# Kernel optimization log

Measured on AMD Instinct MI355X. Metric: run time of the kernel, lower is better.

## Reference

```python
import jax, jax.numpy as jnp
import numpy as np

N_NODES = 50000
N_EDGES = 800000
D = 128            # embedding.hidden_size == sage.hidden_channels
SYN_V, LEM_V, POS_V, SEN_V = 120000, 150000, 5, 210000
LN_EPS = 1e-12


def setup_inputs() -> dict:
    key = jax.random.key(0)
    ks = jax.random.split(key, 12)
    s = 0.02
    inp = {
        "x": jax.random.randint(ks[0], (N_NODES, 4), 0, 5, dtype=jnp.int64)
             if jax.config.jax_enable_x64 else jax.random.randint(ks[0], (N_NODES, 4), 0, 5, dtype=jnp.int32),
        "edge_index": jax.random.randint(ks[1], (2, N_EDGES), 0, N_NODES, dtype=jnp.int32),
        "syn_emb": jax.random.normal(ks[2], (SYN_V, D), jnp.float32) * s,
        "lem_emb": jax.random.normal(ks[3], (LEM_V, D), jnp.float32) * s,
        "pos_emb": jax.random.normal(ks[4], (POS_V, D), jnp.float32) * s,
        "sen_emb": jax.random.normal(ks[5], (SEN_V, D), jnp.float32) * s,
        "ln_g": jnp.ones((D,), jnp.float32),
        "ln_b": jnp.zeros((D,), jnp.float32),
        "Wl0": jax.random.normal(ks[6], (D, D), jnp.float32) * s,
        "bl0": jnp.zeros((D,), jnp.float32),
        "Wr0": jax.random.normal(ks[7], (D, D), jnp.float32) * s,
        "Wl1": jax.random.normal(ks[8], (D, D), jnp.float32) * s,
        "bl1": jnp.zeros((D,), jnp.float32),
        "Wr1": jax.random.normal(ks[9], (D, D), jnp.float32) * s,
    }
    return inp


def _layer_norm(h, g, b):
    mu = jnp.mean(h, axis=-1, keepdims=True)
    var = jnp.mean(jnp.square(h - mu), axis=-1, keepdims=True)
    return (h - mu) * jax.lax.rsqrt(var + LN_EPS) * g + b


def _sage_conv(h, src, dst, Wl, bl, Wr, n_nodes):
    # mean-aggregate source neighbor features at each target node
    msg = h[src]                                            # [E, D] gather
    agg = jax.ops.segment_sum(msg, dst, num_segments=n_nodes)
    cnt = jax.ops.segment_sum(jnp.ones((src.shape[0],), h.dtype), dst,
                              num_segments=n_nodes)
    agg = agg / jnp.maximum(cnt, 1.0)[:, None]              # isolated nodes -> 0
    return agg @ Wl.T + bl + h @ Wr.T                       # lin_l(agg)+lin_r(x)


def reference(x, edge_index, syn_emb, lem_emb, pos_emb, sen_emb, ln_g, ln_b,
              Wl0, bl0, Wr0, Wl1, bl1, Wr1):
    # WordnetEmbeddings: sum of 4 lookups, LayerNorm (dropout = eval identity)
    h = (syn_emb[x[:, 0]] + lem_emb[x[:, 3]]
         + pos_emb[x[:, 1]] + sen_emb[x[:, 2]])
    h = _layer_norm(h, ln_g, ln_b)
    src, dst = edge_index[0], edge_index[1]
    n = h.shape[0]
    # SAGE.full_forward, 2 layers, relu between (dropout = eval identity)
    h = _sage_conv(h, src, dst, Wl0, bl0, Wr0, n)
    h = jax.nn.relu(h)
    h = _sage_conv(h, src, dst, Wl1, bl1, Wr1, n)
    return h
```

## Files before the change

### kernel.cpp

```cpp
#include <hip/hip_runtime.h>

#define D 128
#define LN_EPS 1e-12f

typedef unsigned int uint;
typedef unsigned short ushort_t;
typedef __attribute__((ext_vector_type(8))) short bf16x8;
typedef __attribute__((ext_vector_type(4))) float f32x4;

__device__ inline ushort_t f2bf(float f) {
  uint u = __float_as_uint(f);
  u += 0x7fffu + ((u >> 16) & 1u);
  return (ushort_t)(u >> 16);
}
__device__ inline float bf2f(ushort_t h) {
  return __uint_as_float((uint)h << 16);
}
__device__ inline uint pack_bf16(float a, float b) {
  return (uint)f2bf(a) | ((uint)f2bf(b) << 16);
}

__global__ __launch_bounds__(256) void front_kernel(
    const int* __restrict__ x,
    const float* __restrict__ syn, const float* __restrict__ lem,
    const float* __restrict__ pos, const float* __restrict__ sen,
    const float* __restrict__ g, const float* __restrict__ b,
    ushort_t* __restrict__ hH, ushort_t* __restrict__ hL, int n,
    const int* __restrict__ dst, int* __restrict__ counts, int nEdges,
    const float* __restrict__ Wl0, const float* __restrict__ Wr0,
    const float* __restrict__ Wl1, const float* __restrict__ Wr1,
    ushort_t* __restrict__ Wb0H, ushort_t* __restrict__ Wb0L,
    ushort_t* __restrict__ Wb1H, ushort_t* __restrict__ Wb1L,
    int embB, int histB) {
  int blk = blockIdx.x;
  if (blk >= embB + histB) {
    int idx = (blk - embB - histB) * 256 + threadIdx.x;
    int layer = idx >> 15;
    int e = idx & 32767;
    int col = e >> 8, k = e & 255;
    const float* Wl = layer ? Wl1 : Wl0;
    const float* Wr = layer ? Wr1 : Wr0;
    float v = (k < 128) ? Wl[col * 128 + k] : Wr[col * 128 + (k - 128)];
    ushort_t h = f2bf(v);
    float lo = v - bf2f(h);
    if (layer) {
      Wb1H[e] = h; Wb1L[e] = f2bf(lo);
    } else {
      Wb0H[e] = h; Wb0L[e] = f2bf(lo);
    }
    return;
  }
  if (blk >= embB) {
    int e = (blk - embB) * 256 + threadIdx.x;
    if (e < nEdges) atomicAdd(&counts[dst[e]], 1);
    return;
  }
  int lane = threadIdx.x & 63;
  int q = lane & 31, s = lane >> 5;
  int node = blk * 8 + (threadIdx.x >> 6) * 2 + s;
  if (node >= n) return;
  int4 xi = ((const int4*)x)[node];
  float4 v0 = ((const float4*)(syn + (size_t)xi.x * D))[q];
  float4 v1 = ((const float4*)(pos + (size_t)xi.y * D))[q];
  float4 v2 = ((const float4*)(sen + (size_t)xi.z * D))[q];
  float4 v3 = ((const float4*)(lem + (size_t)xi.w * D))[q];
  float4 hs;
  hs.x = v0.x + v1.x + v2.x + v3.x;
  hs.y = v0.y + v1.y + v2.y + v3.y;
  hs.z = v0.z + v1.z + v2.z + v3.z;
  hs.w = v0.w + v1.w + v2.w + v3.w;
  float sum = hs.x + hs.y + hs.z + hs.w;
#pragma unroll
  for (int off = 16; off; off >>= 1) sum += __shfl_xor(sum, off);
  float mu = sum * (1.0f / 128.0f);
  float4 d;
  d.x = hs.x - mu; d.y = hs.y - mu; d.z = hs.z - mu; d.w = hs.w - mu;
  float sq = d.x * d.x + d.y * d.y + d.z * d.z + d.w * d.w;
#pragma unroll
  for (int off = 16; off; off >>= 1) sq += __shfl_xor(sq, off);
  float rstd = rsqrtf(sq * (1.0f / 128.0f) + LN_EPS);
  float4 gg = ((const float4*)g)[q];
  float4 bb = ((const float4*)b)[q];
  float4 o;
  o.x = d.x * rstd * gg.x + bb.x;
  o.y = d.y * rstd * gg.y + bb.y;
  o.z = d.z * rstd * gg.z + bb.z;
  o.w = d.w * rstd * gg.w + bb.w;
  ushort_t hx = f2bf(o.x), hy = f2bf(o.y), hz = f2bf(o.z), hw = f2bf(o.w);
  uint2 ph;
  ph.x = (uint)hx | ((uint)hy << 16);
  ph.y = (uint)hz | ((uint)hw << 16);
  ((uint2*)(hH + (size_t)node * D))[q] = ph;
  uint2 pl;
  pl.x = pack_bf16(o.x - bf2f(hx), o.y - bf2f(hy));
  pl.y = pack_bf16(o.z - bf2f(hz), o.w - bf2f(hw));
  ((uint2*)(hL + (size_t)node * D))[q] = pl;
}

__global__ __launch_bounds__(256) void scan_part_kernel(
    const int* __restrict__ counts, int* __restrict__ partials) {
  int t = threadIdx.x;
  int base = blockIdx.x * 1024 + t * 4;
  int4 v = *(const int4*)(counts + base);
  int s = v.x + v.y + v.z + v.w;
#pragma unroll
  for (int off = 1; off < 64; off <<= 1) s += __shfl_xor(s, off);
  __shared__ int ws[4];
  if ((t & 63) == 0) ws[t >> 6] = s;
  __syncthreads();
  if (t == 0) partials[blockIdx.x] = ws[0] + ws[1] + ws[2] + ws[3];
}

__global__ __launch_bounds__(256) void scan_write_kernel(
    const int* __restrict__ counts, const int* __restrict__ partials,
    int* __restrict__ row_ptr, int n, int E) {
  int t = threadIdx.x;
  int b = blockIdx.x;
  int off = 0;
  for (int i = 0; i < b; ++i) off += partials[i];
  int base = b * 1024 + t * 4;
  int4 v = *(const int4*)(counts + base);
  int s = v.x + v.y + v.z + v.w;
  int lane = t & 63;
  int incl = s;
#pragma unroll
  for (int dd = 1; dd < 64; dd <<= 1) {
    int u = __shfl_up(incl, dd);
    if (lane >= dd) incl += u;
  }
  __shared__ int wsum[4];
  if (lane == 63) wsum[t >> 6] = incl;
  __syncthreads();
  int wid = t >> 6;
  int wpre = 0;
#pragma unroll
  for (int w = 0; w < 4; ++w)
    if (w < wid) wpre += wsum[w];
  int excl = off + wpre + incl - s;
  int4 r;
  r.x = excl;
  r.y = excl + v.x;
  r.z = r.y + v.y;
  r.w = r.z + v.z;
  if (base + 3 < n) {
    *(int4*)(row_ptr + base) = r;
  } else {
    if (base < n) row_ptr[base] = r.x;
    if (base + 1 < n) row_ptr[base + 1] = r.y;
    if (base + 2 < n) row_ptr[base + 2] = r.z;
    if (base + 3 < n) row_ptr[base + 3] = r.w;
  }
  if (b == 0 && t == 0) row_ptr[n] = E;
}

__global__ __launch_bounds__(256) void fill_kernel(const int* __restrict__ src,
                                                   const int* __restrict__ dst,
                                                   const int* __restrict__ row_ptr,
                                                   int* __restrict__ cursor,
                                                   int* __restrict__ adj,
                                                   int nEdges) {
  int e = blockIdx.x * 256 + threadIdx.x;
  if (e >= nEdges) return;
  int d = dst[e];
  int p = atomicAdd(&cursor[d], 1);
  adj[row_ptr[d] + p] = src[e];
}

__global__ __launch_bounds__(256) void gather_bf16_kernel(
    const int* __restrict__ row_ptr, const int* __restrict__ adj,
    const ushort_t* __restrict__ hb,
    ushort_t* __restrict__ aggH, ushort_t* __restrict__ aggL, int n) {
  int node = blockIdx.x * 4 + (threadIdx.x >> 6);
  if (node >= n) return;
  int lane = threadIdx.x & 63;
  int q = lane & 15, s = lane >> 4;
  int beg = row_ptr[node], end = row_ptr[node + 1];
  int count = end - beg;
  float a0 = 0.f, a1 = 0.f, a2 = 0.f, a3 = 0.f;
  float a4 = 0.f, a5 = 0.f, a6 = 0.f, a7 = 0.f;
  int lim16 = beg + (count & ~15);
  for (int bb = beg; bb < lim16; bb += 16) {
    int e0 = adj[bb + s];
    int e1 = adj[bb + 4 + s];
    int e2 = adj[bb + 8 + s];
    int e3 = adj[bb + 12 + s];
    uint4 v0 = ((const uint4*)(hb + (size_t)e0 * D))[q];
    uint4 v1 = ((const uint4*)(hb + (size_t)e1 * D))[q];
    uint4 v2 = ((const uint4*)(hb + (size_t)e2 * D))[q];
    uint4 v3 = ((const uint4*)(hb + (size_t)e3 * D))[q];
    a0 += __uint_as_float(v0.x << 16) + __uint_as_float(v1.x << 16) +
          __uint_as_float(v2.x << 16) + __uint_as_float(v3.x << 16);
    a1 += __uint_as_float(v0.x & 0xffff0000u) + __uint_as_float(v1.x & 0xffff0000u) +
          __uint_as_float(v2.x & 0xffff0000u) + __uint_as_float(v3.x & 0xffff0000u);
    a2 += __uint_as_float(v0.y << 16) + __uint_as_float(v1.y << 16) +
          __uint_as_float(v2.y << 16) + __uint_as_float(v3.y << 16);
    a3 += __uint_as_float(v0.y & 0xffff0000u) + __uint_as_float(v1.y & 0xffff0000u) +
          __uint_as_float(v2.y & 0xffff0000u) + __uint_as_float(v3.y & 0xffff0000u);
    a4 += __uint_as_float(v0.z << 16) + __uint_as_float(v1.z << 16) +
          __uint_as_float(v2.z << 16) + __uint_as_float(v3.z << 16);
    a5 += __uint_as_float(v0.z & 0xffff0000u) + __uint_as_float(v1.z & 0xffff0000u) +
          __uint_as_float(v2.z & 0xffff0000u) + __uint_as_float(v3.z & 0xffff0000u);
    a6 += __uint_as_float(v0.w << 16) + __uint_as_float(v1.w << 16) +
          __uint_as_float(v2.w << 16) + __uint_as_float(v3.w << 16);
    a7 += __uint_as_float(v0.w & 0xffff0000u) + __uint_as_float(v1.w & 0xffff0000u) +
          __uint_as_float(v2.w & 0xffff0000u) + __uint_as_float(v3.w & 0xffff0000u);
  }
  int p = lim16;
  if (count & 8) {
    int e0 = adj[p + s], e1 = adj[p + 4 + s];
    uint4 v0 = ((const uint4*)(hb + (size_t)e0 * D))[q];
    uint4 v1 = ((const uint4*)(hb + (size_t)e1 * D))[q];
    a0 += __uint_as_float(v0.x << 16) + __uint_as_float(v1.x << 16);
    a1 += __uint_as_float(v0.x & 0xffff0000u) + __uint_as_float(v1.x & 0xffff0000u);
    a2 += __uint_as_float(v0.y << 16) + __uint_as_float(v1.y << 16);
    a3 += __uint_as_float(v0.y & 0xffff0000u) + __uint_as_float(v1.y & 0xffff0000u);
    a4 += __uint_as_float(v0.z << 16) + __uint_as_float(v1.z << 16);
    a5 += __uint_as_float(v0.z & 0xffff0000u) + __uint_as_float(v1.z & 0xffff0000u);
    a6 += __uint_as_float(v0.w << 16) + __uint_as_float(v1.w << 16);
    a7 += __uint_as_float(v0.w & 0xffff0000u) + __uint_as_float(v1.w & 0xffff0000u);
    p += 8;
  }
  for (int i = p + s; i < end; i += 4) {
    int e0 = adj[i];
    uint4 v0 = ((const uint4*)(hb + (size_t)e0 * D))[q];
    a0 += __uint_as_float(v0.x << 16);
    a1 += __uint_as_float(v0.x & 0xffff0000u);
    a2 += __uint_as_float(v0.y << 16);
    a3 += __uint_as_float(v0.y & 0xffff0000u);
    a4 += __uint_as_float(v0.z << 16);
    a5 += __uint_as_float(v0.z & 0xffff0000u);
    a6 += __uint_as_float(v0.w << 16);
    a7 += __uint_as_float(v0.w & 0xffff0000u);
  }
#pragma unroll
  for (int off = 16; off <= 32; off <<= 1) {
    a0 += __shfl_xor(a0, off); a1 += __shfl_xor(a1, off);
    a2 += __shfl_xor(a2, off); a3 += __shfl_xor(a3, off);
    a4 += __shfl_xor(a4, off); a5 += __shfl_xor(a5, off);
    a6 += __shfl_xor(a6, off); a7 += __shfl_xor(a7, off);
  }
  if (s == 0) {
    float inv = 1.0f / fmaxf((float)count, 1.0f);
    float v0 = a0 * inv, v1 = a1 * inv, v2 = a2 * inv, v3 = a3 * inv;
    float v4 = a4 * inv, v5 = a5 * inv, v6 = a6 * inv, v7 = a7 * inv;
    ushort_t h0 = f2bf(v0), h1 = f2bf(v1), h2 = f2bf(v2), h3 = f2bf(v3);
    ushort_t h4 = f2bf(v4), h5 = f2bf(v5), h6 = f2bf(v6), h7 = f2bf(v7);
    uint4 ph;
    ph.x = (uint)h0 | ((uint)h1 << 16);
    ph.y = (uint)h2 | ((uint)h3 << 16);
    ph.z = (uint)h4 | ((uint)h5 << 16);
    ph.w = (uint)h6 | ((uint)h7 << 16);
    uint4 pl;
    pl.x = pack_bf16(v0 - bf2f(h0), v1 - bf2f(h1));
    pl.y = pack_bf16(v2 - bf2f(h2), v3 - bf2f(h3));
    pl.z = pack_bf16(v4 - bf2f(h4), v5 - bf2f(h5));
    pl.w = pack_bf16(v6 - bf2f(h6), v7 - bf2f(h7));
    *(uint4*)(aggH + (size_t)node * D + q * 8) = ph;
    *(uint4*)(aggL + (size_t)node * D + q * 8) = pl;
  }
}

__global__ __launch_bounds__(256) void sage_mfma_kernel(
    const ushort_t* __restrict__ aggH, const ushort_t* __restrict__ aggL,
    const ushort_t* hinH, const ushort_t* hinL,
    const ushort_t* __restrict__ WbH, const ushort_t* __restrict__ WbL,
    const float* __restrict__ bias,
    float* outF, ushort_t* outH, ushort_t* outL, int n, int doRelu) {
  __shared__ ushort_t AsH[128 * 64];
  __shared__ ushort_t AsL[128 * 64];
  __shared__ ushort_t BsH[128 * 64];
  __shared__ ushort_t BsL[128 * 64];
  int tid = threadIdx.x;
  int lane = tid & 63;
  int wave = tid >> 6;
  int base = blockIdx.x * 128;
  int wr = (wave & 1) * 64;
  int wc = (wave >> 1) * 64;

  f32x4 zero = {0.f, 0.f, 0.f, 0.f};
  f32x4 acc[4][4];
#pragma unroll
  for (int i = 0; i < 4; ++i)
#pragma unroll
    for (int j = 0; j < 4; ++j) acc[i][j] = zero;

  int row = tid >> 1;
  int half = tid & 1;
  int kb0 = half * 64;
  int swz = (row & 7) << 4;
  char* aHdst = (char*)AsH + row * 128;
  char* aLdst = (char*)AsL + row * 128;
  char* bHdst = (char*)BsH + row * 128;
  char* bLdst = (char*)BsL + row * 128;
  int anode = base + row;
  if (anode >= n) anode = n - 1;
  const ushort_t* wHsrc = WbH + (size_t)row * 256 + half * 32;
  const ushort_t* wLsrc = WbL + (size_t)row * 256 + half * 32;

  for (int kc = 0; kc < 4; ++kc) {
    {
      const ushort_t* sH = (kc < 2 ? aggH : hinH) +
                           (size_t)anode * D + (kc & 1) * 64 + half * 32;
      const ushort_t* sL = (kc < 2 ? aggL : hinL) +
                           (size_t)anode * D + (kc & 1) * 64 + half * 32;
      uint4 h0 = *(const uint4*)sH;
      uint4 h1 = *(const uint4*)(sH + 8);
      uint4 h2 = *(const uint4*)(sH + 16);
      uint4 h3 = *(const uint4*)(sH + 24);
      uint4 l0 = *(const uint4*)sL;
      uint4 l1 = *(const uint4*)(sL + 8);
      uint4 l2 = *(const uint4*)(sL + 16);
      uint4 l3 = *(const uint4*)(sL + 24);
      *(uint4*)(aHdst + ((kb0) ^ swz)) = h0;
      *(uint4*)(aHdst + ((kb0 + 16) ^ swz)) = h1;
      *(uint4*)(aHdst + ((kb0 + 32) ^ swz)) = h2;
      *(uint4*)(aHdst + ((kb0 + 48) ^ swz)) = h3;
      *(uint4*)(aLdst + ((kb0) ^ swz)) = l0;
      *(uint4*)(aLdst + ((kb0 + 16) ^ swz)) = l1;
      *(uint4*)(aLdst + ((kb0 + 32) ^ swz)) = l2;
      *(uint4*)(aLdst + ((kb0 + 48) ^ swz)) = l3;
    }
    {
      const ushort_t* sH = wHsrc + kc * 64;
      const ushort_t* sL = wLsrc + kc * 64;
      uint4 h0 = *(const uint4*)sH;
      uint4 h1 = *(const uint4*)(sH + 8);
      uint4 h2 = *(const uint4*)(sH + 16);
      uint4 h3 = *(const uint4*)(sH + 24);
      uint4 l0 = *(const uint4*)sL;
      uint4 l1 = *(const uint4*)(sL + 8);
      uint4 l2 = *(const uint4*)(sL + 16);
      uint4 l3 = *(const uint4*)(sL + 24);
      *(uint4*)(bHdst + ((kb0) ^ swz)) = h0;
      *(uint4*)(bHdst + ((kb0 + 16) ^ swz)) = h1;
      *(uint4*)(bHdst + ((kb0 + 32) ^ swz)) = h2;
      *(uint4*)(bHdst + ((kb0 + 48) ^ swz)) = h3;
      *(uint4*)(bLdst + ((kb0) ^ swz)) = l0;
      *(uint4*)(bLdst + ((kb0 + 16) ^ swz)) = l1;
      *(uint4*)(bLdst + ((kb0 + 32) ^ swz)) = l2;
      *(uint4*)(bLdst + ((kb0 + 48) ^ swz)) = l3;
    }
    __syncthreads();
#pragma unroll
    for (int ks = 0; ks < 2; ++ks) {
      int kb = ks * 64 + (lane >> 4) * 16;
      bf16x8 aHf[4], aLf[4], bHf[4], bLf[4];
#pragma unroll
      for (int rf = 0; rf < 4; ++rf) {
        int r = wr + rf * 16 + (lane & 15);
        int off = r * 128 + (kb ^ ((r & 7) << 4));
        aHf[rf] = *(const bf16x8*)((const char*)AsH + off);
        aLf[rf] = *(const bf16x8*)((const char*)AsL + off);
      }
#pragma unroll
      for (int cf = 0; cf < 4; ++cf) {
        int c = wc + cf * 16 + (lane & 15);
        int off = c * 128 + (kb ^ ((c & 7) << 4));
        bHf[cf] = *(const bf16x8*)((const char*)BsH + off);
        bLf[cf] = *(const bf16x8*)((const char*)BsL + off);
      }
#pragma unroll
      for (int rf = 0; rf < 4; ++rf)
#pragma unroll
        for (int cf = 0; cf < 4; ++cf) {
          acc[rf][cf] = __builtin_amdgcn_mfma_f32_16x16x32_bf16(
              aHf[rf], bHf[cf], acc[rf][cf], 0, 0, 0);
          acc[rf][cf] = __builtin_amdgcn_mfma_f32_16x16x32_bf16(
              aHf[rf], bLf[cf], acc[rf][cf], 0, 0, 0);
          acc[rf][cf] = __builtin_amdgcn_mfma_f32_16x16x32_bf16(
              aLf[rf], bHf[cf], acc[rf][cf], 0, 0, 0);
        }
    }
    __syncthreads();
  }

#pragma unroll
  for (int cf = 0; cf < 4; ++cf) {
    int j = wc + cf * 16 + (lane & 15);
    float bj = bias[j];
#pragma unroll
    for (int rf = 0; rf < 4; ++rf) {
      int r0 = base + wr + rf * 16 + (lane >> 4) * 4;
#pragma unroll
      for (int reg = 0; reg < 4; ++reg) {
        int node = r0 + reg;
        if (node >= n) continue;
        float v = acc[rf][cf][reg] + bj;
        if (doRelu) v = fmaxf(v, 0.f);
        if (outF) outF[(size_t)node * D + j] = v;
        if (outH) {
          ushort_t h = f2bf(v);
          outH[(size_t)node * D + j] = h;
          outL[(size_t)node * D + j] = f2bf(v - bf2f(h));
        }
      }
    }
  }
}

extern "C" void kernel_launch(void* const* d_in, const int* in_sizes, int n_in,
                              void* d_out, int out_size, void* d_ws,
                              size_t ws_size, hipStream_t stream) {
  const int* x = (const int*)d_in[0];
  const int* edge = (const int*)d_in[1];
  const float* syn = (const float*)d_in[2];
  const float* lem = (const float*)d_in[3];
  const float* pos = (const float*)d_in[4];
  const float* sen = (const float*)d_in[5];
  const float* ln_g = (const float*)d_in[6];
  const float* ln_b = (const float*)d_in[7];
  const float* Wl0 = (const float*)d_in[8];
  const float* bl0 = (const float*)d_in[9];
  const float* Wr0 = (const float*)d_in[10];
  const float* Wl1 = (const float*)d_in[11];
  const float* bl1 = (const float*)d_in[12];
  const float* Wr1 = (const float*)d_in[13];

  int n = in_sizes[0] / 4;
  int E = in_sizes[1] / 2;
  const int* srcI = edge;
  const int* dstI = edge + E;
  float* outp = (float*)d_out;

  size_t rowElems = (size_t)n * D;
  int nPad = (n + 1023) & ~1023;
  int scanBlocks = nPad >> 10;
  int rpElems = (n + 4) & ~3;
  ushort_t* h0H = (ushort_t*)d_ws;
  ushort_t* h0L = h0H + rowElems;
  ushort_t* aggH = h0L + rowElems;
  ushort_t* aggL = aggH + rowElems;
  ushort_t* Wb0H = aggL + rowElems;
  ushort_t* Wb0L = Wb0H + 32768;
  ushort_t* Wb1H = Wb0L + 32768;
  ushort_t* Wb1L = Wb1H + 32768;
  int* row_ptr = (int*)(Wb1L + 32768);
  int* counts = row_ptr + rpElems;
  int* cursor = counts + nPad;
  int* partials = cursor + n;
  int* adj = partials + scanBlocks;

  hipMemsetAsync(counts, 0, ((size_t)nPad + n) * sizeof(int), stream);

  int embB = (n + 7) / 8;
  int histB = (E + 255) / 256;
  front_kernel<<<embB + histB + 256, 256, 0, stream>>>(
      x, syn, lem, pos, sen, ln_g, ln_b, h0H, h0L, n,
      dstI, counts, E,
      Wl0, Wr0, Wl1, Wr1, Wb0H, Wb0L, Wb1H, Wb1L,
      embB, histB);

  scan_part_kernel<<<scanBlocks, 256, 0, stream>>>(counts, partials);
  scan_write_kernel<<<scanBlocks, 256, 0, stream>>>(counts, partials, row_ptr,
                                                    n, E);
  fill_kernel<<<histB, 256, 0, stream>>>(srcI, dstI, row_ptr, cursor, adj, E);

  int gBlocks = (n + 3) / 4;
  int sBlocks = (n + 127) / 128;

  gather_bf16_kernel<<<gBlocks, 256, 0, stream>>>(row_ptr, adj, h0H, aggH,
                                                  aggL, n);
  sage_mfma_kernel<<<sBlocks, 256, 0, stream>>>(aggH, aggL, h0H, h0L, Wb0H,
                                                Wb0L, bl0, nullptr, h0H, h0L,
                                                n, 1);
  gather_bf16_kernel<<<gBlocks, 256, 0, stream>>>(row_ptr, adj, h0H, aggH,
                                                  aggL, n);
  sage_mfma_kernel<<<sBlocks, 256, 0, stream>>>(aggH, aggL, h0H, h0L, Wb1H,
                                                Wb1L, bl1, outp, nullptr,
                                                nullptr, n, 0);
}
```

Before: 421.9 us.

## Reuse histogram atomic rank in CSR fill and load MFMA tiles via global_load_lds

The histogram pass now records each edge's atomic return value as its rank. The fill kernel then places each edge using row_ptr plus that rank, which removes the second atomic pass and the cursor memset. The SAGE MFMA kernel stages its A and B tiles with direct global-to-LDS 16-byte loads instead of going through registers, keeping the same XOR swizzle. This costs an extra E-sized rank buffer in global memory and depends on the swizzled slot mapping matching the fragment reads exactly.

```diff
diff --git a/kernel.cpp b/kernel.cpp
--- a/kernel.cpp
+++ b/kernel.cpp
@@ -7,6 +7,12 @@
 typedef unsigned short ushort_t;
 typedef __attribute__((ext_vector_type(8))) short bf16x8;
 typedef __attribute__((ext_vector_type(4))) float f32x4;
+
+typedef const __attribute__((address_space(1))) void gvoid_t;
+typedef __attribute__((address_space(3))) void lvoid_t;
+__device__ __forceinline__ void gl_lds16(const void* g, void* l) {
+  __builtin_amdgcn_global_load_lds((gvoid_t*)g, (lvoid_t*)l, 16, 0, 0);
+}
 
 __device__ inline ushort_t f2bf(float f) {
   uint u = __float_as_uint(f);
@@ -26,7 +32,8 @@
     const float* __restrict__ pos, const float* __restrict__ sen,
     const float* __restrict__ g, const float* __restrict__ b,
     ushort_t* __restrict__ hH, ushort_t* __restrict__ hL, int n,
-    const int* __restrict__ dst, int* __restrict__ counts, int nEdges,
+    const int* __restrict__ dst, int* __restrict__ counts,
+    int* __restrict__ rank, int nEdges,
     const float* __restrict__ Wl0, const float* __restrict__ Wr0,
     const float* __restrict__ Wl1, const float* __restrict__ Wr1,
     ushort_t* __restrict__ Wb0H, ushort_t* __restrict__ Wb0L,
@@ -52,7 +59,7 @@
   }
   if (blk >= embB) {
     int e = (blk - embB) * 256 + threadIdx.x;
-    if (e < nEdges) atomicAdd(&counts[dst[e]], 1);
+    if (e < nEdges) rank[e] = atomicAdd(&counts[dst[e]], 1);
     return;
   }
   int lane = threadIdx.x & 63;
@@ -156,14 +163,13 @@
 __global__ __launch_bounds__(256) void fill_kernel(const int* __restrict__ src,
                                                    const int* __restrict__ dst,
                                                    const int* __restrict__ row_ptr,
-                                                   int* __restrict__ cursor,
+                                                   const int* __restrict__ rank,
                                                    int* __restrict__ adj,
                                                    int nEdges) {
   int e = blockIdx.x * 256 + threadIdx.x;
   if (e >= nEdges) return;
   int d = dst[e];
-  int p = atomicAdd(&cursor[d], 1);
-  adj[row_ptr[d] + p] = src[e];
+  adj[row_ptr[d] + rank[e]] = src[e];
 }
 
 __global__ __launch_bounds__(256) void gather_bf16_kernel(
@@ -284,61 +290,26 @@
 #pragma unroll
     for (int j = 0; j < 4; ++j) acc[i][j] = zero;
 
-  int row = tid >> 1;
-  int half = tid & 1;
-  int kb0 = half * 64;
-  int swz = (row & 7) << 4;
-  char* aHdst = (char*)AsH + row * 128;
-  char* aLdst = (char*)AsL + row * 128;
-  char* bHdst = (char*)BsH + row * 128;
-  char* bLdst = (char*)BsL + row * 128;
-  int anode = base + row;
-  if (anode >= n) anode = n - 1;
-  const ushort_t* wHsrc = WbH + (size_t)row * 256 + half * 32;
-  const ushort_t* wLsrc = WbL + (size_t)row * 256 + half * 32;
-
   for (int kc = 0; kc < 4; ++kc) {
-    {
-      const ushort_t* sH = (kc < 2 ? aggH : hinH) +
-                           (size_t)anode * D + (kc & 1) * 64 + half * 32;
-      const ushort_t* sL = (kc < 2 ? aggL : hinL) +
-                           (size_t)anode * D + (kc & 1) * 64 + half * 32;
-      uint4 h0 = *(const uint4*)sH;
-      uint4 h1 = *(const uint4*)(sH + 8);
-      uint4 h2 = *(const uint4*)(sH + 16);
-      uint4 h3 = *(const uint4*)(sH + 24);
-      uint4 l0 = *(const uint4*)sL;
-      uint4 l1 = *(const uint4*)(sL + 8);
-      uint4 l2 = *(const uint4*)(sL + 16);
-      uint4 l3 = *(const uint4*)(sL + 24);
-      *(uint4*)(aHdst + ((kb0) ^ swz)) = h0;
-      *(uint4*)(aHdst + ((kb0 + 16) ^ swz)) = h1;
-      *(uint4*)(aHdst + ((kb0 + 32) ^ swz)) = h2;
-      *(uint4*)(aHdst + ((kb0 + 48) ^ swz)) = h3;
-      *(uint4*)(aLdst + ((kb0) ^ swz)) = l0;
-      *(uint4*)(aLdst + ((kb0 + 16) ^ swz)) = l1;
-      *(uint4*)(aLdst + ((kb0 + 32) ^ swz)) = l2;
-      *(uint4*)(aLdst + ((kb0 + 48) ^ swz)) = l3;
-    }
-    {
-      const ushort_t* sH = wHsrc + kc * 64;
-      const ushort_t* sL = wLsrc + kc * 64;
-      uint4 h0 = *(const uint4*)sH;
-      uint4 h1 = *(const uint4*)(sH + 8);
-      uint4 h2 = *(const uint4*)(sH + 16);
-      uint4 h3 = *(const uint4*)(sH + 24);
-      uint4 l0 = *(const uint4*)sL;
-      uint4 l1 = *(const uint4*)(sL + 8);
-      uint4 l2 = *(const uint4*)(sL + 16);
-      uint4 l3 = *(const uint4*)(sL + 24);
-      *(uint4*)(bHdst + ((kb0) ^ swz)) = h0;
-      *(uint4*)(bHdst + ((kb0 + 16) ^ swz)) = h1;
-      *(uint4*)(bHdst + ((kb0 + 32) ^ swz)) = h2;
-      *(uint4*)(bHdst + ((kb0 + 48) ^ swz)) = h3;
-      *(uint4*)(bLdst + ((kb0) ^ swz)) = l0;
-      *(uint4*)(bLdst + ((kb0 + 16) ^ swz)) = l1;
-      *(uint4*)(bLdst + ((kb0 + 32) ^ swz)) = l2;
-      *(uint4*)(bLdst + ((kb0 + 48) ^ swz)) = l3;
+    const char* aH = (const char*)((kc < 2) ? aggH : hinH);
+    const char* aL = (const char*)((kc < 2) ? aggL : hinL);
+    int aoff = (kc & 1) * 128;
+    int boff = kc * 128;
+#pragma unroll
+    for (int i = 0; i < 4; ++i) {
+      int grp = i * 4 + wave;
+      int slot = grp * 64 + lane;
+      int row = slot >> 3;
+      int cs = ((slot & 7) * 16) ^ ((row & 7) << 4);
+      int anode = base + row;
+      if (anode >= n) anode = n - 1;
+      size_t abyte = (size_t)anode * 256 + aoff + cs;
+      size_t bbyte = (size_t)row * 512 + boff + cs;
+      uint ldsb = (uint)grp * 1024;
+      gl_lds16(aH + abyte, (char*)AsH + ldsb);
+      gl_lds16(aL + abyte, (char*)AsL + ldsb);
+      gl_lds16((const char*)WbH + bbyte, (char*)BsH + ldsb);
+      gl_lds16((const char*)WbL + bbyte, (char*)BsL + ldsb);
     }
     __syncthreads();
 #pragma unroll
@@ -436,24 +407,24 @@
   ushort_t* Wb1L = Wb1H + 32768;
   int* row_ptr = (int*)(Wb1L + 32768);
   int* counts = row_ptr + rpElems;
-  int* cursor = counts + nPad;
-  int* partials = cursor + n;
+  int* rank = counts + nPad;
+  int* partials = rank + E;
   int* adj = partials + scanBlocks;
 
-  hipMemsetAsync(counts, 0, ((size_t)nPad + n) * sizeof(int), stream);
+  hipMemsetAsync(counts, 0, (size_t)nPad * sizeof(int), stream);
 
   int embB = (n + 7) / 8;
   int histB = (E + 255) / 256;
   front_kernel<<<embB + histB + 256, 256, 0, stream>>>(
       x, syn, lem, pos, sen, ln_g, ln_b, h0H, h0L, n,
-      dstI, counts, E,
+      dstI, counts, rank, E,
       Wl0, Wr0, Wl1, Wr1, Wb0H, Wb0L, Wb1H, Wb1L,
       embB, histB);
 
   scan_part_kernel<<<scanBlocks, 256, 0, stream>>>(counts, partials);
   scan_write_kernel<<<scanBlocks, 256, 0, stream>>>(counts, partials, row_ptr,
                                                     n, E);
-  fill_kernel<<<histB, 256, 0, stream>>>(srcI, dstI, row_ptr, cursor, adj, E);
+  fill_kernel<<<histB, 256, 0, stream>>>(srcI, dstI, row_ptr, rank, adj, E);
 
   int gBlocks = (n + 3) / 4;
   int sBlocks = (n + 127) / 128;
```

After: 407.7 us. -3.4%, faster.
